# Optimization experiments

Measured on AMD Instinct MI355X. Metric: run time of the kernel, lower is better.

## Reference

```python
import jax, jax.numpy as jnp
import numpy as np

MODEL_DIM = 1024
NUM_HEADS = 16
HEAD_DIM = MODEL_DIM // NUM_HEADS
EPS = 1e-12
CHUNK = 128  # chunk size for the linear-attention recurrence


def setup_inputs() -> dict:
    key = jax.random.key(0)
    kx, kq, kk, kv, ko = jax.random.split(key, 5)
    b, l = 4, 4096
    x = jax.random.normal(kx, (b, l, MODEL_DIM), dtype=jnp.float32)
    # nn.Linear weights, init std=0.02, no bias; torch Linear computes x @ W.T
    Wq = 0.02 * jax.random.normal(kq, (MODEL_DIM, MODEL_DIM), dtype=jnp.float32)
    Wk = 0.02 * jax.random.normal(kk, (MODEL_DIM, MODEL_DIM), dtype=jnp.float32)
    Wv = 0.02 * jax.random.normal(kv, (MODEL_DIM, MODEL_DIM), dtype=jnp.float32)
    Wo = 0.02 * jax.random.normal(ko, (MODEL_DIM, MODEL_DIM), dtype=jnp.float32)
    return {"x": x, "Wq": Wq, "Wk": Wk, "Wv": Wv, "Wo": Wo}


def _pos_elu(t):
    # feature_map = F.elu(x) + 1
    return jax.nn.elu(t) + 1.0


def _linear_attention(q, k, v):
    # q,k,v: (b,h,l,d) with feature map already applied.
    # Causal linear attention: out_t = (q_t . sum_{s<=t} k_s v_s^T) / (q_t . sum_{s<=t} k_s) + EPS
    # Chunked recurrence over the (d,d) KV state avoids the (b,h,l,d,d) cumsum.
    b, h, l, d = q.shape
    nc = l // CHUNK
    qc = jnp.moveaxis(q.reshape(b, h, nc, CHUNK, d), 2, 0)  # (nc,b,h,C,d)
    kc = jnp.moveaxis(k.reshape(b, h, nc, CHUNK, d), 2, 0)
    vc = jnp.moveaxis(v.reshape(b, h, nc, CHUNK, d), 2, 0)
    mask = jnp.tril(jnp.ones((CHUNK, CHUNK), dtype=q.dtype))  # causal within chunk

    def step(carry, inp):
        S, z = carry  # S:(b,h,d,d) running sum k v^T; z:(b,h,d) running sum k
        qb, kb, vb = inp  # (b,h,C,d)
        scores = jnp.einsum('bhcd,bhsd->bhcs', qb, kb) * mask  # (b,h,C,C)
        num = jnp.einsum('bhcd,bhde->bhce', qb, S) + jnp.einsum('bhcs,bhse->bhce', scores, vb)
        den = jnp.einsum('bhcd,bhd->bhc', qb, z) + scores.sum(-1)  # (b,h,C)
        out = num / den[..., None] + EPS  # NOTE: eps added after division, as in source
        S = S + jnp.einsum('bhsd,bhse->bhde', kb, vb)
        z = z + kb.sum(axis=2)
        return (S, z), out

    S0 = jnp.zeros((b, h, d, d), dtype=q.dtype)
    z0 = jnp.zeros((b, h, d), dtype=q.dtype)
    _, outs = jax.lax.scan(step, (S0, z0), (qc, kc, vc))  # (nc,b,h,C,d)
    # -> (b, l, h, d)
    return jnp.moveaxis(outs, 0, 1).transpose(0, 3, 1, 2, 4).reshape(b, h * 0 + l // l, 0, 0) if False else outs


def reference(x, Wq, Wk, Wv, Wo):
    b, l, D = x.shape
    h, d = NUM_HEADS, HEAD_DIM
    # projections (torch Linear: x @ W.T), split heads -> (b,h,l,d)
    q = (x @ Wq.T).reshape(b, l, h, d).transpose(0, 2, 1, 3)
    k = (x @ Wk.T).reshape(b, l, h, d).transpose(0, 2, 1, 3)
    v = (x @ Wv.T).reshape(b, l, h, d).transpose(0, 2, 1, 3)
    q = _pos_elu(q)
    k = _pos_elu(k)
    outs = _linear_attention(q, k, v)  # (nc,b,h,C,d)
    nc = l // CHUNK
    # (nc,b,h,C,d) -> (b,nc,C,h,d) -> (b,l,D)  (matches transpose(1,2).view in torch)
    attn = outs.transpose(1, 0, 3, 2, 4).reshape(b, l, D)
    return attn @ Wo.T
```

## Files before the change

kernel.cpp:

```cpp
#include <hip/hip_runtime.h>
#include <stdint.h>

typedef float f32x4 __attribute__((ext_vector_type(4)));
typedef __bf16 bf16x8 __attribute__((ext_vector_type(8)));
typedef unsigned short u16x8 __attribute__((ext_vector_type(8)));

#define DEV __device__ __forceinline__

DEV unsigned short f2bf(float f) {
  unsigned int u = __float_as_uint(f);
  unsigned int r = (u + 0x7FFFu + ((u >> 16) & 1u)) >> 16;
  return (unsigned short)r;
}
DEV float b2f(unsigned short h) { return __uint_as_float(((unsigned int)h) << 16); }

DEV void gload16(const void* g, void* l) {
  __builtin_amdgcn_global_load_lds((__attribute__((address_space(1))) void*)(g),
                                   (__attribute__((address_space(3))) void*)(l), 16, 0, 0);
}

__global__ void cast_all(const float* __restrict__ x, const float* __restrict__ Wq,
                         const float* __restrict__ Wk, const float* __restrict__ Wv,
                         const float* __restrict__ Wo, unsigned short* __restrict__ xbf,
                         unsigned short* __restrict__ wqkv, unsigned short* __restrict__ wo) {
  int i = blockIdx.x * 256 + threadIdx.x;
  const float* src;
  unsigned short* dst;
  int j;
  if (i < 2097152) {
    src = x; dst = xbf; j = i;
  } else {
    int k = i - 2097152;
    int sel = k >> 17; j = k & 131071;
    src = (sel == 0) ? Wq : (sel == 1) ? Wk : (sel == 2) ? Wv : Wo;
    dst = (sel < 3) ? (wqkv + (size_t)sel * 1048576) : wo;
  }
  const float4* p = (const float4*)src + (size_t)j * 2;
  float4 a = p[0], b = p[1];
  u16x8 o;
  o[0] = f2bf(a.x); o[1] = f2bf(a.y); o[2] = f2bf(a.z); o[3] = f2bf(a.w);
  o[4] = f2bf(b.x); o[5] = f2bf(b.y); o[6] = f2bf(b.z); o[7] = f2bf(b.w);
  ((u16x8*)dst)[j] = o;
}

template<int MODE>
__global__ __launch_bounds__(256, 2) void gemm_bt(
    const unsigned short* __restrict__ A, const unsigned short* __restrict__ Bw,
    void* __restrict__ out0, unsigned short* __restrict__ qp,
    unsigned short* __restrict__ kp, unsigned short* __restrict__ vp,
    int K, int N, int nTn)
{
  __shared__ unsigned short sA[128 * 64];
  __shared__ unsigned short sB[128 * 64];
  int t = threadIdx.x, w = t >> 6, lane = t & 63, fr = lane & 15, fq = lane >> 4;
  int bid = blockIdx.x;
  int bm = bid / nTn, bn = bid % nTn;
  int wm = w >> 1, wn = w & 1;

  f32x4 acc[4][4];
  f32x4 z4 = {0.f, 0.f, 0.f, 0.f};
#pragma unroll
  for (int mi = 0; mi < 4; ++mi)
#pragma unroll
    for (int ni = 0; ni < 4; ++ni) acc[mi][ni] = z4;

  for (int k0 = 0; k0 < K; k0 += 64) {
#pragma unroll
    for (int i = 0; i < 4; ++i) {
      int p = (i * 4 + w) * 64 + lane;
      int r = p >> 3;
      int c8 = (p & 7) ^ (r & 7);
      gload16(A + (size_t)(bm * 128 + r) * K + k0 + c8 * 8, &sA[(i * 4 + w) * 512]);
      gload16(Bw + (size_t)(bn * 128 + r) * K + k0 + c8 * 8, &sB[(i * 4 + w) * 512]);
    }
    __syncthreads();
#pragma unroll
    for (int ks = 0; ks < 2; ++ks) {
      bf16x8 af[4], bg[4];
#pragma unroll
      for (int mi = 0; mi < 4; ++mi) {
        int r = wm * 64 + mi * 16 + fr;
        int c8 = (ks * 4 + fq) ^ (r & 7);
        af[mi] = *(const bf16x8*)&sA[(r * 8 + c8) * 8];
      }
#pragma unroll
      for (int ni = 0; ni < 4; ++ni) {
        int r = wn * 64 + ni * 16 + fr;
        int c8 = (ks * 4 + fq) ^ (r & 7);
        bg[ni] = *(const bf16x8*)&sB[(r * 8 + c8) * 8];
      }
#pragma unroll
      for (int mi = 0; mi < 4; ++mi)
#pragma unroll
        for (int ni = 0; ni < 4; ++ni)
          acc[mi][ni] = __builtin_amdgcn_mfma_f32_16x16x32_bf16(af[mi], bg[ni], acc[mi][ni], 0, 0, 0);
    }
    __syncthreads();
  }

  if (MODE == 0) {
    float* O = (float*)out0;
#pragma unroll
    for (int mi = 0; mi < 4; ++mi)
#pragma unroll
      for (int ni = 0; ni < 4; ++ni)
#pragma unroll
        for (int j = 0; j < 4; ++j) {
          int m = bm * 128 + wm * 64 + mi * 16 + fq * 4 + j;
          int n = bn * 128 + wn * 64 + ni * 16 + fr;
          O[(size_t)m * N + n] = acc[mi][ni][j];
        }
  } else {
    int tsel = (bn * 128) >> 10;
    unsigned short* base = (tsel == 0) ? qp : ((tsel == 1) ? kp : vp);
#pragma unroll
    for (int mi = 0; mi < 4; ++mi)
#pragma unroll
      for (int ni = 0; ni < 4; ++ni)
#pragma unroll
        for (int j = 0; j < 4; ++j) {
          int m = bm * 128 + wm * 64 + mi * 16 + fq * 4 + j;
          int n = bn * 128 + wn * 64 + ni * 16 + fr;
          int col1 = n & 1023;
          int h = col1 >> 6, d = col1 & 63;
          int b = m >> 12, l = m & 4095;
          float v = acc[mi][ni][j];
          if (tsel < 2) v = (v > 0.f) ? (v + 1.f) : __expf(v);
          base[(((size_t)(b * 16 + h)) * 4096 + l) * 64 + d] = f2bf(v);
        }
  }
}

__global__ __launch_bounds__(256) void chunk_state(
    const unsigned short* __restrict__ kb, const unsigned short* __restrict__ vb,
    unsigned short* __restrict__ Spref, float* __restrict__ zbuf)
{
  __shared__ unsigned short kT[64 * 136];
  __shared__ unsigned short vT[64 * 136];
  int t = threadIdx.x, w = t >> 6, lane = t & 63, fr = lane & 15, fq = lane >> 4;
  int bh = blockIdx.x >> 5, c = blockIdx.x & 31;
  size_t base = ((size_t)bh * 4096 + (size_t)c * 128) * 64;

  int s = t >> 1, d0 = (t & 1) * 32;
  const unsigned short* kpp = kb + base + (size_t)s * 64 + d0;
  const unsigned short* vpp = vb + base + (size_t)s * 64 + d0;
#pragma unroll
  for (int i = 0; i < 4; ++i) {
    u16x8 kr = *(const u16x8*)(kpp + i * 8);
    u16x8 vr = *(const u16x8*)(vpp + i * 8);
#pragma unroll
    for (int j = 0; j < 8; ++j) {
      int d = d0 + i * 8 + j;
      kT[d * 136 + s] = kr[j];
      vT[d * 136 + s] = vr[j];
    }
  }
  __syncthreads();

  f32x4 acc[4];
  f32x4 z4 = {0.f, 0.f, 0.f, 0.f};
#pragma unroll
  for (int n = 0; n < 4; ++n) acc[n] = z4;
#pragma unroll
  for (int ks = 0; ks < 4; ++ks) {
    bf16x8 av = *(const bf16x8*)&vT[(w * 16 + fr) * 136 + ks * 32 + fq * 8];
#pragma unroll
    for (int n = 0; n < 4; ++n) {
      bf16x8 bk = *(const bf16x8*)&kT[(n * 16 + fr) * 136 + ks * 32 + fq * 8];
      acc[n] = __builtin_amdgcn_mfma_f32_16x16x32_bf16(av, bk, acc[n], 0, 0, 0);
    }
  }
  size_t ob = ((size_t)bh * 32 + c) * 4096;
#pragma unroll
  for (int n = 0; n < 4; ++n)
#pragma unroll
    for (int j = 0; j < 4; ++j) {
      int e = w * 16 + fq * 4 + j, dd = n * 16 + fr;
      Spref[ob + (size_t)e * 64 + dd] = f2bf(acc[n][j]);
    }
  if (t < 64) {
    float z = 0.f;
#pragma unroll
    for (int i = 0; i < 16; ++i) {
      u16x8 kr = *(const u16x8*)&kT[t * 136 + i * 8];
#pragma unroll
      for (int j = 0; j < 8; ++j) z += b2f(kr[j]);
    }
    zbuf[((size_t)bh * 32 + c) * 64 + t] = z;
  }
}

__global__ __launch_bounds__(256) void scan_all(
    unsigned short* __restrict__ Spref, const float* __restrict__ zbuf,
    float* __restrict__ zpref)
{
  if (blockIdx.x < 512) {
    int idx = blockIdx.x * 256 + threadIdx.x;
    int bh = idx >> 11, i = idx & 2047;
    unsigned int* p32 = (unsigned int*)Spref;
    size_t base = (size_t)bh * 32 * 2048 + i;
    float r0 = 0.f, r1 = 0.f;
#pragma unroll
    for (int c = 0; c < 32; ++c) {
      unsigned int v = p32[base + (size_t)c * 2048];
      float v0 = b2f((unsigned short)(v & 0xFFFFu));
      float v1 = b2f((unsigned short)(v >> 16));
      p32[base + (size_t)c * 2048] =
          (unsigned int)f2bf(r0) | ((unsigned int)f2bf(r1) << 16);
      r0 += v0; r1 += v1;
    }
  } else {
    int idx = (blockIdx.x - 512) * 256 + threadIdx.x;
    size_t base = (size_t)(idx >> 6) * 32 * 64 + (idx & 63);
    float run = 0.f;
#pragma unroll
    for (int c = 0; c < 32; ++c) {
      float v = zbuf[base + c * 64];
      zpref[base + c * 64] = run;
      run += v;
    }
  }
}

__global__ __launch_bounds__(256, 2) void chunk_out(
    const unsigned short* __restrict__ qb, const unsigned short* __restrict__ kb,
    const unsigned short* __restrict__ vb, const unsigned short* __restrict__ Spref,
    const float* __restrict__ zpref, unsigned short* __restrict__ attn)
{
  __shared__ unsigned short sq[128 * 64];
  __shared__ unsigned short skv[128 * 64];
  __shared__ unsigned short ss[128 * 128];
  __shared__ unsigned short sS[80 * 64];
  int t = threadIdx.x, w = t >> 6, lane = t & 63, fr = lane & 15, fq = lane >> 4;
  int bh = blockIdx.x >> 5, c = blockIdx.x & 31;
  size_t qkbase = ((size_t)bh * 4096 + (size_t)c * 128) * 64;
  size_t sbase = ((size_t)bh * 32 + c) * 4096;

  u16x8 vreg[4];
#pragma unroll
  for (int i = 0; i < 4; ++i)
    vreg[i] = *(const u16x8*)(vb + qkbase + (size_t)(t * 4 + i) * 8);

#pragma unroll
  for (int i = 0; i < 4; ++i) {
    int p = t * 4 + i, r = p >> 3, c8 = p & 7;
    int sw = (r * 8 + (c8 ^ (r & 7))) * 8;
    *(u16x8*)&sq[sw] = *(const u16x8*)(qb + qkbase + (size_t)p * 8);
    *(u16x8*)&skv[sw] = *(const u16x8*)(kb + qkbase + (size_t)p * 8);
  }
#pragma unroll
  for (int i = 0; i < 2; ++i) {
    int p = t * 2 + i, e = p >> 3, c8 = p & 7;
    *(u16x8*)&sS[(e * 8 + (c8 ^ (e & 7))) * 8] = *(const u16x8*)(Spref + sbase + (size_t)p * 8);
  }
  if (t < 64) sS[64 * 64 + t] = f2bf(zpref[((size_t)bh * 32 + c) * 64 + t]);
  {
    unsigned int* zz = (unsigned int*)&sS[65 * 64];
    for (int i = t; i < 480; i += 256) zz[i] = 0u;
  }
  __syncthreads();

  int rowbase = w * 32;
  bf16x8 aq[2][2];
#pragma unroll
  for (int mi = 0; mi < 2; ++mi)
#pragma unroll
    for (int kt = 0; kt < 2; ++kt) {
      int r = rowbase + mi * 16 + fr;
      int c8 = (kt * 4 + fq) ^ (r & 7);
      aq[mi][kt] = *(const bf16x8*)&sq[(r * 8 + c8) * 8];
    }

  f32x4 accsT[2][8];
  f32x4 z4 = {0.f, 0.f, 0.f, 0.f};
#pragma unroll
  for (int mi = 0; mi < 2; ++mi)
#pragma unroll
    for (int ni = 0; ni < 8; ++ni) accsT[mi][ni] = z4;

#pragma unroll
  for (int ni = 0; ni < 8; ++ni)
#pragma unroll
    for (int kt = 0; kt < 2; ++kt) {
      int r = ni * 16 + fr;
      int c8 = (kt * 4 + fq) ^ (r & 7);
      bf16x8 bk = *(const bf16x8*)&skv[(r * 8 + c8) * 8];
      accsT[0][ni] = __builtin_amdgcn_mfma_f32_16x16x32_bf16(bk, aq[0][kt], accsT[0][ni], 0, 0, 0);
      accsT[1][ni] = __builtin_amdgcn_mfma_f32_16x16x32_bf16(bk, aq[1][kt], accsT[1][ni], 0, 0, 0);
    }

  float rs[2];
#pragma unroll
  for (int mi = 0; mi < 2; ++mi) {
    int m16 = mi * 16 + fr;
    float sum = 0.f;
#pragma unroll
    for (int ni = 0; ni < 8; ++ni)
#pragma unroll
      for (int j = 0; j < 4; ++j) {
        int s = ni * 16 + fq * 4 + j - rowbase;
        float v = (s <= m16) ? accsT[mi][ni][j] : 0.f;
        accsT[mi][ni][j] = v;
        sum += v;
      }
    sum += __shfl_xor(sum, 16, 64);
    sum += __shfl_xor(sum, 32, 64);
    rs[mi] = sum;
  }
  __syncthreads();

#pragma unroll
  for (int i = 0; i < 4; ++i) {
    int p = t * 4 + i, s = p >> 3, e0g = (p & 7) * 8;
#pragma unroll
    for (int j = 0; j < 8; ++j) {
      int e = e0g + j;
      skv[(e * 16 + ((s >> 3) ^ (e & 15))) * 8 + (s & 7)] = vreg[i][j];
    }
  }
#pragma unroll
  for (int mi = 0; mi < 2; ++mi) {
    int m = rowbase + mi * 16 + fr;
#pragma unroll
    for (int ni = 0; ni < 8; ++ni)
#pragma unroll
      for (int p = 0; p < 2; ++p) {
        unsigned int pk = (unsigned int)f2bf(accsT[mi][ni][2 * p]) |
                          ((unsigned int)f2bf(accsT[mi][ni][2 * p + 1]) << 16);
        int chunk = (2 * ni + (fq >> 1)) ^ (m & 15);
        *(unsigned int*)&ss[m * 128 + chunk * 8 + (fq & 1) * 4 + 2 * p] = pk;
      }
  }
  __syncthreads();

  f32x4 acco[2][4];
  f32x4 accd[2];
#pragma unroll
  for (int mi = 0; mi < 2; ++mi) {
    accd[mi] = z4;
#pragma unroll
    for (int ni = 0; ni < 4; ++ni) acco[mi][ni] = z4;
  }
#pragma unroll
  for (int kt = 0; kt < 2; ++kt) {
#pragma unroll
    for (int ni = 0; ni < 4; ++ni) {
      int r = ni * 16 + fr;
      int c8 = (kt * 4 + fq) ^ (r & 7);
      bf16x8 bS = *(const bf16x8*)&sS[(r * 8 + c8) * 8];
      acco[0][ni] = __builtin_amdgcn_mfma_f32_16x16x32_bf16(aq[0][kt], bS, acco[0][ni], 0, 0, 0);
      acco[1][ni] = __builtin_amdgcn_mfma_f32_16x16x32_bf16(aq[1][kt], bS, acco[1][ni], 0, 0, 0);
    }
    {
      int r = 64 + fr;
      int c8 = (kt * 4 + fq) ^ (r & 7);
      bf16x8 bz = *(const bf16x8*)&sS[(r * 8 + c8) * 8];
      accd[0] = __builtin_amdgcn_mfma_f32_16x16x32_bf16(aq[0][kt], bz, accd[0], 0, 0, 0);
      accd[1] = __builtin_amdgcn_mfma_f32_16x16x32_bf16(aq[1][kt], bz, accd[1], 0, 0, 0);
    }
  }
#pragma unroll
  for (int kt = 0; kt < 4; ++kt) {
    bf16x8 am[2];
#pragma unroll
    for (int mi = 0; mi < 2; ++mi) {
      int r = rowbase + mi * 16 + fr;
      int c8 = (kt * 4 + fq) ^ (r & 15);
      am[mi] = *(const bf16x8*)&ss[(r * 16 + c8) * 8];
    }
#pragma unroll
    for (int ni = 0; ni < 4; ++ni) {
      int r = ni * 16 + fr;
      int c8 = (kt * 4 + fq) ^ (r & 15);
      bf16x8 bv = *(const bf16x8*)&skv[(r * 16 + c8) * 8];
      acco[0][ni] = __builtin_amdgcn_mfma_f32_16x16x32_bf16(am[0], bv, acco[0][ni], 0, 0, 0);
      acco[1][ni] = __builtin_amdgcn_mfma_f32_16x16x32_bf16(am[1], bv, acco[1][ni], 0, 0, 0);
    }
  }

  int b = bh >> 4, h = bh & 15;
#pragma unroll
  for (int mi = 0; mi < 2; ++mi)
#pragma unroll
    for (int j = 0; j < 4; ++j) {
      float rsj = __shfl(rs[mi], fq * 4 + j, 64);
      float den = __shfl(accd[mi][j], (lane & 48), 64) + rsj;
      float rden = 1.f / den;
      int m = rowbase + mi * 16 + fq * 4 + j;
      size_t rowoff = ((size_t)b * 4096 + (size_t)c * 128 + m) * 1024 + h * 64;
#pragma unroll
      for (int ni = 0; ni < 4; ++ni) {
        int e = ni * 16 + fr;
        float o = acco[mi][ni][j] * rden + 1e-12f;
        attn[rowoff + e] = f2bf(o);
      }
    }
}

extern "C" void kernel_launch(void* const* d_in, const int* in_sizes, int n_in,
                              void* d_out, int out_size, void* d_ws, size_t ws_size,
                              hipStream_t stream) {
  (void)in_sizes; (void)n_in; (void)out_size; (void)ws_size;
  const float* x = (const float*)d_in[0];
  const float* Wq = (const float*)d_in[1];
  const float* Wk = (const float*)d_in[2];
  const float* Wv = (const float*)d_in[3];
  const float* Wo = (const float*)d_in[4];
  char* ws = (char*)d_ws;
  unsigned short* xbf  = (unsigned short*)(ws + 0);
  unsigned short* wqkv = (unsigned short*)(ws + 33554432);
  unsigned short* wo   = (unsigned short*)(ws + 39845888);
  unsigned short* q    = (unsigned short*)(ws + 41943040);
  unsigned short* k    = (unsigned short*)(ws + 75497472);
  unsigned short* v    = (unsigned short*)(ws + 109051904);
  unsigned short* attn = (unsigned short*)(ws + 142606336);
  unsigned short* Spref= (unsigned short*)(ws + 176160768);
  float* zbuf          = (float*)(ws + 192937984);
  float* zpref         = (float*)(ws + 193462272);

  cast_all<<<10240, 256, 0, stream>>>(x, Wq, Wk, Wv, Wo, xbf, wqkv, wo);
  gemm_bt<1><<<3072, 256, 0, stream>>>(xbf, wqkv, nullptr, q, k, v, 1024, 3072, 24);
  chunk_state<<<2048, 256, 0, stream>>>(k, v, Spref, zbuf);
  scan_all<<<528, 256, 0, stream>>>(Spref, zbuf, zpref);
  chunk_out<<<2048, 256, 0, stream>>>(q, k, v, Spref, zpref, attn);
  gemm_bt<0><<<1024, 256, 0, stream>>>(attn, wo, d_out, nullptr, nullptr, nullptr, 1024, 1024, 8);
}
```

Baseline: 227.8 us.

## Store V pre-transposed and swizzled per chunk from the QKV GEMM epilogue

The QKV GEMM epilogue for the V columns now transposes its tile through shared memory and writes V in a per-chunk, transposed, XOR-swizzled layout with coalesced 16-byte stores. chunk_state and chunk_out load this layout straight into LDS with global_load_lds, so they no longer do scalar per-element transposes of V in shared memory. chunk_out reuses the q buffer for V after Q is held in registers, which costs an extra barrier. This spreads V layout work across three kernels and adds an LDS round trip plus a barrier to the GEMM epilogue.

```diff
diff --git a/kernel.cpp b/kernel.cpp
--- a/kernel.cpp
+++ b/kernel.cpp
@@ -47,11 +47,12 @@
 __global__ __launch_bounds__(256, 2) void gemm_bt(
     const unsigned short* __restrict__ A, const unsigned short* __restrict__ Bw,
     void* __restrict__ out0, unsigned short* __restrict__ qp,
-    unsigned short* __restrict__ kp, unsigned short* __restrict__ vp,
+    unsigned short* __restrict__ kp, unsigned short* __restrict__ vtg,
     int K, int N, int nTn)
 {
-  __shared__ unsigned short sA[128 * 64];
-  __shared__ unsigned short sB[128 * 64];
+  __shared__ unsigned short sAB[2 * 128 * 64];
+  unsigned short* sA = sAB;
+  unsigned short* sB = sAB + 8192;
   int t = threadIdx.x, w = t >> 6, lane = t & 63, fr = lane & 15, fq = lane >> 4;
   int bid = blockIdx.x;
   int bm = bid / nTn, bn = bid % nTn;
@@ -112,48 +113,74 @@
         }
   } else {
     int tsel = (bn * 128) >> 10;
-    unsigned short* base = (tsel == 0) ? qp : ((tsel == 1) ? kp : vp);
-#pragma unroll
-    for (int mi = 0; mi < 4; ++mi)
-#pragma unroll
-      for (int ni = 0; ni < 4; ++ni)
-#pragma unroll
-        for (int j = 0; j < 4; ++j) {
-          int m = bm * 128 + wm * 64 + mi * 16 + fq * 4 + j;
-          int n = bn * 128 + wn * 64 + ni * 16 + fr;
-          int col1 = n & 1023;
-          int h = col1 >> 6, d = col1 & 63;
-          int b = m >> 12, l = m & 4095;
-          float v = acc[mi][ni][j];
-          if (tsel < 2) v = (v > 0.f) ? (v + 1.f) : __expf(v);
-          base[(((size_t)(b * 16 + h)) * 4096 + l) * 64 + d] = f2bf(v);
-        }
+    if (tsel < 2) {
+      unsigned short* base = (tsel == 0) ? qp : kp;
+#pragma unroll
+      for (int mi = 0; mi < 4; ++mi)
+#pragma unroll
+        for (int ni = 0; ni < 4; ++ni)
+#pragma unroll
+          for (int j = 0; j < 4; ++j) {
+            int m = bm * 128 + wm * 64 + mi * 16 + fq * 4 + j;
+            int n = bn * 128 + wn * 64 + ni * 16 + fr;
+            int col1 = n & 1023;
+            int h = col1 >> 6, d = col1 & 63;
+            int b = m >> 12, l = m & 4095;
+            float v = acc[mi][ni][j];
+            v = (v > 0.f) ? (v + 1.f) : __expf(v);
+            base[(((size_t)(b * 16 + h)) * 4096 + l) * 64 + d] = f2bf(v);
+          }
+    } else {
+      unsigned short* vbuf = sAB;
+#pragma unroll
+      for (int mi = 0; mi < 4; ++mi)
+#pragma unroll
+        for (int ni = 0; ni < 4; ++ni)
+#pragma unroll
+          for (int j = 0; j < 4; ++j) {
+            int r = wn * 64 + ni * 16 + fr;
+            int m_l = wm * 64 + mi * 16 + fq * 4 + j;
+            int mc = m_l >> 3;
+            vbuf[r * 128 + ((mc ^ (r & 7)) << 3) + (m_l & 7)] = f2bf(acc[mi][ni][j]);
+          }
+      __syncthreads();
+      int b2 = bm >> 5, cch = bm & 31;
+      int h0 = (bn - 16) * 2;
+#pragma unroll
+      for (int i = 0; i < 8; ++i) {
+        int f = (i * 4 + w) * 64 + lane;
+        int hsel = f >> 10;
+        int ff = f & 1023;
+        size_t gb = ((size_t)((b2 * 16 + h0 + hsel) * 32 + cch)) * 8192 + (size_t)ff * 8;
+        *(u16x8*)(vtg + gb) = *(const u16x8*)&vbuf[f * 8];
+      }
+    }
   }
 }
 
 __global__ __launch_bounds__(256) void chunk_state(
-    const unsigned short* __restrict__ kb, const unsigned short* __restrict__ vb,
+    const unsigned short* __restrict__ kb, const unsigned short* __restrict__ vtg,
     unsigned short* __restrict__ Spref, float* __restrict__ zbuf)
 {
   __shared__ unsigned short kT[64 * 136];
-  __shared__ unsigned short vT[64 * 136];
+  __shared__ unsigned short vT[64 * 128];
   int t = threadIdx.x, w = t >> 6, lane = t & 63, fr = lane & 15, fq = lane >> 4;
   int bh = blockIdx.x >> 5, c = blockIdx.x & 31;
   size_t base = ((size_t)bh * 4096 + (size_t)c * 128) * 64;
-
+  const unsigned short* vsrc = vtg + ((size_t)bh * 32 + c) * 8192;
+
+#pragma unroll
+  for (int i = 0; i < 4; ++i) {
+    int g = i * 4 + w;
+    gload16(vsrc + (size_t)(g * 64 + lane) * 8, &vT[g * 512]);
+  }
   int s = t >> 1, d0 = (t & 1) * 32;
   const unsigned short* kpp = kb + base + (size_t)s * 64 + d0;
-  const unsigned short* vpp = vb + base + (size_t)s * 64 + d0;
 #pragma unroll
   for (int i = 0; i < 4; ++i) {
     u16x8 kr = *(const u16x8*)(kpp + i * 8);
-    u16x8 vr = *(const u16x8*)(vpp + i * 8);
-#pragma unroll
-    for (int j = 0; j < 8; ++j) {
-      int d = d0 + i * 8 + j;
-      kT[d * 136 + s] = kr[j];
-      vT[d * 136 + s] = vr[j];
-    }
+#pragma unroll
+    for (int j = 0; j < 8; ++j) kT[(d0 + i * 8 + j) * 136 + s] = kr[j];
   }
   __syncthreads();
 
@@ -163,7 +190,8 @@
   for (int n = 0; n < 4; ++n) acc[n] = z4;
 #pragma unroll
   for (int ks = 0; ks < 4; ++ks) {
-    bf16x8 av = *(const bf16x8*)&vT[(w * 16 + fr) * 136 + ks * 32 + fq * 8];
+    int r = w * 16 + fr;
+    bf16x8 av = *(const bf16x8*)&vT[r * 128 + (((ks * 4 + fq) ^ (r & 7)) << 3)];
 #pragma unroll
     for (int n = 0; n < 4; ++n) {
       bf16x8 bk = *(const bf16x8*)&kT[(n * 16 + fr) * 136 + ks * 32 + fq * 8];
@@ -224,10 +252,10 @@
 
 __global__ __launch_bounds__(256, 2) void chunk_out(
     const unsigned short* __restrict__ qb, const unsigned short* __restrict__ kb,
-    const unsigned short* __restrict__ vb, const unsigned short* __restrict__ Spref,
+    const unsigned short* __restrict__ vtg, const unsigned short* __restrict__ Spref,
     const float* __restrict__ zpref, unsigned short* __restrict__ attn)
 {
-  __shared__ unsigned short sq[128 * 64];
+  __shared__ unsigned short squ[128 * 64];
   __shared__ unsigned short skv[128 * 64];
   __shared__ unsigned short ss[128 * 128];
   __shared__ unsigned short sS[80 * 64];
@@ -235,17 +263,13 @@
   int bh = blockIdx.x >> 5, c = blockIdx.x & 31;
   size_t qkbase = ((size_t)bh * 4096 + (size_t)c * 128) * 64;
   size_t sbase = ((size_t)bh * 32 + c) * 4096;
-
-  u16x8 vreg[4];
-#pragma unroll
-  for (int i = 0; i < 4; ++i)
-    vreg[i] = *(const u16x8*)(vb + qkbase + (size_t)(t * 4 + i) * 8);
+  const unsigned short* vsrc = vtg + ((size_t)bh * 32 + c) * 8192;
 
 #pragma unroll
   for (int i = 0; i < 4; ++i) {
     int p = t * 4 + i, r = p >> 3, c8 = p & 7;
     int sw = (r * 8 + (c8 ^ (r & 7))) * 8;
-    *(u16x8*)&sq[sw] = *(const u16x8*)(qb + qkbase + (size_t)p * 8);
+    *(u16x8*)&squ[sw] = *(const u16x8*)(qb + qkbase + (size_t)p * 8);
     *(u16x8*)&skv[sw] = *(const u16x8*)(kb + qkbase + (size_t)p * 8);
   }
 #pragma unroll
@@ -268,8 +292,15 @@
     for (int kt = 0; kt < 2; ++kt) {
       int r = rowbase + mi * 16 + fr;
       int c8 = (kt * 4 + fq) ^ (r & 7);
-      aq[mi][kt] = *(const bf16x8*)&sq[(r * 8 + c8) * 8];
-    }
+      aq[mi][kt] = *(const bf16x8*)&squ[(r * 8 + c8) * 8];
+    }
+  __syncthreads();
+
+#pragma unroll
+  for (int i = 0; i < 4; ++i) {
+    int g = i * 4 + w;
+    gload16(vsrc + (size_t)(g * 64 + lane) * 8, &squ[g * 512]);
+  }
 
   f32x4 accsT[2][8];
   f32x4 z4 = {0.f, 0.f, 0.f, 0.f};
@@ -307,17 +338,7 @@
     sum += __shfl_xor(sum, 32, 64);
     rs[mi] = sum;
   }
-  __syncthreads();
-
-#pragma unroll
-  for (int i = 0; i < 4; ++i) {
-    int p = t * 4 + i, s = p >> 3, e0g = (p & 7) * 8;
-#pragma unroll
-    for (int j = 0; j < 8; ++j) {
-      int e = e0g + j;
-      skv[(e * 16 + ((s >> 3) ^ (e & 15))) * 8 + (s & 7)] = vreg[i][j];
-    }
-  }
+
 #pragma unroll
   for (int mi = 0; mi < 2; ++mi) {
     int m = rowbase + mi * 16 + fr;
@@ -371,8 +392,7 @@
 #pragma unroll
     for (int ni = 0; ni < 4; ++ni) {
       int r = ni * 16 + fr;
-      int c8 = (kt * 4 + fq) ^ (r & 15);
-      bf16x8 bv = *(const bf16x8*)&skv[(r * 16 + c8) * 8];
+      bf16x8 bv = *(const bf16x8*)&squ[r * 128 + (((kt * 4 + fq) ^ (r & 7)) << 3)];
       acco[0][ni] = __builtin_amdgcn_mfma_f32_16x16x32_bf16(am[0], bv, acco[0][ni], 0, 0, 0);
       acco[1][ni] = __builtin_amdgcn_mfma_f32_16x16x32_bf16(am[1], bv, acco[1][ni], 0, 0, 0);
     }
@@ -412,16 +432,16 @@
   unsigned short* wo   = (unsigned short*)(ws + 39845888);
   unsigned short* q    = (unsigned short*)(ws + 41943040);
   unsigned short* k    = (unsigned short*)(ws + 75497472);
-  unsigned short* v    = (unsigned short*)(ws + 109051904);
+  unsigned short* vt   = (unsigned short*)(ws + 109051904);
   unsigned short* attn = (unsigned short*)(ws + 142606336);
   unsigned short* Spref= (unsigned short*)(ws + 176160768);
   float* zbuf          = (float*)(ws + 192937984);
   float* zpref         = (float*)(ws + 193462272);
 
   cast_all<<<10240, 256, 0, stream>>>(x, Wq, Wk, Wv, Wo, xbf, wqkv, wo);
-  gemm_bt<1><<<3072, 256, 0, stream>>>(xbf, wqkv, nullptr, q, k, v, 1024, 3072, 24);
-  chunk_state<<<2048, 256, 0, stream>>>(k, v, Spref, zbuf);
+  gemm_bt<1><<<3072, 256, 0, stream>>>(xbf, wqkv, nullptr, q, k, vt, 1024, 3072, 24);
+  chunk_state<<<2048, 256, 0, stream>>>(k, vt, Spref, zbuf);
   scan_all<<<528, 256, 0, stream>>>(Spref, zbuf, zpref);
-  chunk_out<<<2048, 256, 0, stream>>>(q, k, v, Spref, zpref, attn);
+  chunk_out<<<2048, 256, 0, stream>>>(q, k, vt, Spref, zpref, attn);
   gemm_bt<0><<<1024, 256, 0, stream>>>(attn, wo, d_out, nullptr, nullptr, nullptr, 1024, 1024, 8);
 }
```

Result: no change. 229.6 us (+0.8%).
